# Kernel optimization log

Hardware: AMD Instinct MI355X
Metric: run time of the kernel (lower is better)

## Reference

```python
import jax, jax.numpy as jnp
import numpy as np

TEMP = 0.1        # ds_temperature
THRESHOLD = 0.2
MARGIN = 2        # margin_remove


def setup_inputs() -> dict:
    key = jax.random.key(0)
    k0, k1 = jax.random.split(key)
    N, C = 2, 256
    h0, w0, h1, w1 = 60, 80, 60, 80
    feature0 = jax.random.normal(k0, (N, h0 * w0, C), dtype=jnp.float32)
    feature1 = jax.random.normal(k1, (N, h1 * w1, C), dtype=jnp.float32)
    return {"feature0": feature0, "feature1": feature1,
            "h0": h0, "w0": w0, "h1": h1, "w1": w1}


def _interior(n: int, b: int) -> jnp.ndarray:
    # True on [b, n-b), mirroring mask[:, :b]=False and mask[:, -b:]=False
    a = jnp.arange(n)
    return (a >= b) & (a < n - b)


def reference(feature0, feature1, h0, w0, h1, w1):
    N, L, C = feature0.shape
    S = feature1.shape[1]
    # similarities: (f0/sqrt(C)) . (f1/sqrt(C)) / temp == f0.f1 / (C*temp)
    sim = jnp.einsum('nlc,nsc->nls', feature0, feature1) / (C * TEMP)
    # dual softmax confidences
    conf = jax.nn.softmax(sim, axis=2) * jax.nn.softmax(sim, axis=1)
    # threshold mask with spatial margin removal (mask0 is None branch)
    mask = conf > THRESHOLD                      # [N, L, S]
    m5 = mask.reshape(N, h0, w0, h1, w1)
    valid = (_interior(h0, MARGIN)[:, None, None, None]
             & _interior(w0, MARGIN)[None, :, None, None]
             & _interior(h1, MARGIN)[None, None, :, None]
             & _interior(w1, MARGIN)[None, None, None, :])
    m5 = m5 & valid[None]
    mask = m5.reshape(N, L, S)
    # mutual nearest neighbor constraint
    mutual = ((conf == conf.max(axis=2, keepdims=True))
              & (conf == conf.max(axis=1, keepdims=True)))
    mask = mask & mutual
    # dense (jit-safe) encoding of the matches: confidences zeroed off-match.
    matched_conf = jnp.where(mask, conf, 0.0)
    return conf, mask, matched_conf
```

## Files before the change

### kernel.cpp

```cpp
#include <hip/hip_runtime.h>

#define NB 2
#define LD 4800
#define SD 4800
#define CD 256
#define H0 60
#define W0 80
#define H1 60
#define W1 80
#define MG 2
#define THRESH 0.2f
#define SIM_SCALE (1.0f / (256.0f * 0.1f))
#define GT 38

typedef float f32x4 __attribute__((ext_vector_type(4)));
typedef __bf16 bf16x8 __attribute__((ext_vector_type(8)));
typedef unsigned short u16x8 __attribute__((ext_vector_type(8)));

#define GLOBAL_AS __attribute__((address_space(1)))
#define LDS_AS __attribute__((address_space(3)))

__device__ __forceinline__ void gl_lds16(const unsigned short* g, unsigned short* l) {
    __builtin_amdgcn_global_load_lds((const GLOBAL_AS unsigned int*)g,
                                     (LDS_AS unsigned int*)l, 16, 0, 0);
}

__device__ __forceinline__ unsigned short f2bf(float f) {
    unsigned int u = __float_as_uint(f);
    u = u + 0x7FFFu + ((u >> 16) & 1u);
    return (unsigned short)(u >> 16);
}

__device__ __forceinline__ bool interior0(int idx) {
    int i = idx / W0, j = idx % W0;
    return (i >= MG) & (i < H0 - MG) & (j >= MG) & (j < W0 - MG);
}
__device__ __forceinline__ bool interior1(int idx) {
    int i = idx / W1, j = idx % W1;
    return (i >= MG) & (i < H1 - MG) & (j >= MG) & (j < W1 - MG);
}

__global__ __launch_bounds__(256) void k_zero(float* __restrict__ p, int n) {
    int i = blockIdx.x * 256 + threadIdx.x;
    if (i < n) p[i] = 0.f;
}

__global__ __launch_bounds__(256) void k_cvt(const float* __restrict__ src,
                                             unsigned short* __restrict__ dst, int n8) {
    int i = blockIdx.x * 256 + threadIdx.x;
    if (i >= n8) return;
    const float4* s = (const float4*)src + (size_t)i * 2;
    float4 a = s[0], b = s[1];
    u16x8 o = {f2bf(a.x), f2bf(a.y), f2bf(a.z), f2bf(a.w),
               f2bf(b.x), f2bf(b.y), f2bf(b.z), f2bf(b.w)};
    *(u16x8*)(dst + (size_t)i * 8) = o;
}

template <int PASS>
__global__ __launch_bounds__(256) void k_gemm(const unsigned short* __restrict__ bA,
                                              const unsigned short* __restrict__ bB,
                                              float* __restrict__ rowsum,
                                              float* __restrict__ colsum,
                                              float* __restrict__ conf,
                                              unsigned int* __restrict__ rowmax,
                                              unsigned int* __restrict__ colmax) {
    __shared__ __align__(16) unsigned short As[128][32];
    __shared__ __align__(16) unsigned short Bs[128][32];

    const int n  = blockIdx.z;
    const int s0 = blockIdx.x * 128;
    const int l0 = blockIdx.y * 128;
    const int tid  = threadIdx.x;
    const int lane = tid & 63;
    const int wave = tid >> 6;
    const int wm = (wave >> 1) * 64;
    const int wn = (wave & 1) * 64;
    const int quad = lane >> 4;
    const int lr   = lane & 15;

    const int sr = wave * 32 + (lane >> 2);
    const int sc = (lane & 3) * 8;
    const unsigned short* ga0 = bA + ((size_t)n * LD + min(l0 + sr,      LD - 1)) * CD + sc;
    const unsigned short* ga1 = bA + ((size_t)n * LD + min(l0 + sr + 16, LD - 1)) * CD + sc;
    const unsigned short* gb0 = bB + ((size_t)n * SD + min(s0 + sr,      SD - 1)) * CD + sc;
    const unsigned short* gb1 = bB + ((size_t)n * SD + min(s0 + sr + 16, SD - 1)) * CD + sc;
    unsigned short* la0 = &As[wave * 32][0];
    unsigned short* la1 = &As[wave * 32 + 16][0];
    unsigned short* lb0 = &Bs[wave * 32][0];
    unsigned short* lb1 = &Bs[wave * 32 + 16][0];

    f32x4 acc[4][4];
#pragma unroll
    for (int i = 0; i < 4; ++i)
#pragma unroll
        for (int j = 0; j < 4; ++j) acc[i][j] = (f32x4){0.f, 0.f, 0.f, 0.f};

    for (int k0 = 0; k0 < CD; k0 += 32) {
        __syncthreads();
        gl_lds16(ga0 + k0, la0);
        gl_lds16(ga1 + k0, la1);
        gl_lds16(gb0 + k0, lb0);
        gl_lds16(gb1 + k0, lb1);
        __syncthreads();

        bf16x8 af[4], bfr[4];
#pragma unroll
        for (int i = 0; i < 4; ++i) {
            af[i]  = __builtin_bit_cast(bf16x8, *(const u16x8*)&As[wm + i * 16 + lr][quad * 8]);
            bfr[i] = __builtin_bit_cast(bf16x8, *(const u16x8*)&Bs[wn + i * 16 + lr][quad * 8]);
        }
#pragma unroll
        for (int i = 0; i < 4; ++i)
#pragma unroll
            for (int j = 0; j < 4; ++j)
                acc[i][j] = __builtin_amdgcn_mfma_f32_16x16x32_bf16(af[i], bfr[j], acc[i][j], 0, 0, 0);
    }

    const int rb = l0 + wm;
    const int cb = s0 + wn;

    if (PASS == 0) {
        float rpart[4][4];
        float cpart[4];
#pragma unroll
        for (int i = 0; i < 4; ++i) {
            cpart[i] = 0.f;
#pragma unroll
            for (int g = 0; g < 4; ++g) rpart[i][g] = 0.f;
        }
#pragma unroll
        for (int mi = 0; mi < 4; ++mi)
#pragma unroll
            for (int ni = 0; ni < 4; ++ni)
#pragma unroll
                for (int g = 0; g < 4; ++g) {
                    int row = rb + mi * 16 + quad * 4 + g;
                    int col = cb + ni * 16 + lr;
                    float sv = acc[mi][ni][g] * SIM_SCALE;
                    bool ok = (row < LD) & (col < SD);
                    float ev = ok ? __expf(sv) : 0.f;
                    rpart[mi][g] += ev;
                    cpart[ni] += ev;
                }
#pragma unroll
        for (int mi = 0; mi < 4; ++mi)
#pragma unroll
            for (int g = 0; g < 4; ++g) {
                float v = rpart[mi][g];
                v += __shfl_xor(v, 1);
                v += __shfl_xor(v, 2);
                v += __shfl_xor(v, 4);
                v += __shfl_xor(v, 8);
                int row = rb + mi * 16 + quad * 4 + g;
                if (lr == 0 && row < LD) atomicAdd(&rowsum[n * LD + row], v);
            }
#pragma unroll
        for (int ni = 0; ni < 4; ++ni) {
            float v = cpart[ni];
            v += __shfl_xor(v, 16);
            v += __shfl_xor(v, 32);
            int col = cb + ni * 16 + lr;
            if (quad == 0 && col < SD) atomicAdd(&colsum[n * SD + col], v);
        }
    } else {
        float rinv[4][4], cinv[4];
#pragma unroll
        for (int mi = 0; mi < 4; ++mi)
#pragma unroll
            for (int g = 0; g < 4; ++g) {
                int row = min(rb + mi * 16 + quad * 4 + g, LD - 1);
                rinv[mi][g] = 1.0f / rowsum[n * LD + row];
            }
#pragma unroll
        for (int ni = 0; ni < 4; ++ni) {
            int col = min(cb + ni * 16 + lr, SD - 1);
            cinv[ni] = 1.0f / colsum[n * SD + col];
        }
        float rmx[4][4], cmx[4];
#pragma unroll
        for (int i = 0; i < 4; ++i) {
            cmx[i] = 0.f;
#pragma unroll
            for (int g = 0; g < 4; ++g) rmx[i][g] = 0.f;
        }
#pragma unroll
        for (int mi = 0; mi < 4; ++mi)
#pragma unroll
            for (int ni = 0; ni < 4; ++ni)
#pragma unroll
                for (int g = 0; g < 4; ++g) {
                    int row = rb + mi * 16 + quad * 4 + g;
                    int col = cb + ni * 16 + lr;
                    float sv = acc[mi][ni][g] * SIM_SCALE;
                    float e = __expf(sv);
                    float cv = e * e * rinv[mi][g] * cinv[ni];
                    bool ok = (row < LD) & (col < SD);
                    if (ok) {
                        conf[((size_t)n * LD + row) * SD + col] = cv;
                        rmx[mi][g] = fmaxf(rmx[mi][g], cv);
                        cmx[ni]    = fmaxf(cmx[ni], cv);
                    }
                }
#pragma unroll
        for (int mi = 0; mi < 4; ++mi)
#pragma unroll
            for (int g = 0; g < 4; ++g) {
                float v = rmx[mi][g];
                v = fmaxf(v, __shfl_xor(v, 1));
                v = fmaxf(v, __shfl_xor(v, 2));
                v = fmaxf(v, __shfl_xor(v, 4));
                v = fmaxf(v, __shfl_xor(v, 8));
                int row = rb + mi * 16 + quad * 4 + g;
                if (lr == 0 && row < LD)
                    atomicMax(&rowmax[n * LD + row], __float_as_uint(v));
            }
#pragma unroll
        for (int ni = 0; ni < 4; ++ni) {
            float v = cmx[ni];
            v = fmaxf(v, __shfl_xor(v, 16));
            v = fmaxf(v, __shfl_xor(v, 32));
            int col = cb + ni * 16 + lr;
            if (quad == 0 && col < SD)
                atomicMax(&colmax[n * SD + col], __float_as_uint(v));
        }
    }
}

__global__ __launch_bounds__(256) void k_final(const float* __restrict__ conf,
                                               const float* __restrict__ rowmax,
                                               const float* __restrict__ colmax,
                                               float* __restrict__ mask,
                                               float* __restrict__ matched) {
    const int l = blockIdx.x, n = blockIdx.y;
    const size_t base = ((size_t)n * LD + l) * SD;
    const bool v0 = interior0(l);
    const float rm = rowmax[n * LD + l];
    const float* cm = colmax + (size_t)n * SD;
    for (int s = threadIdx.x * 4; s < SD; s += 1024) {
        float4 c = *(const float4*)(conf + base + s);
        float4 x = *(const float4*)(cm + s);
        float4 mk, mt;
        {
            bool b = v0 & (c.x > THRESH) & interior1(s + 0) & (c.x == rm) & (c.x == x.x);
            mk.x = b ? 1.f : 0.f; mt.x = b ? c.x : 0.f;
        }
        {
            bool b = v0 & (c.y > THRESH) & interior1(s + 1) & (c.y == rm) & (c.y == x.y);
            mk.y = b ? 1.f : 0.f; mt.y = b ? c.y : 0.f;
        }
        {
            bool b = v0 & (c.z > THRESH) & interior1(s + 2) & (c.z == rm) & (c.z == x.z);
            mk.z = b ? 1.f : 0.f; mt.z = b ? c.z : 0.f;
        }
        {
            bool b = v0 & (c.w > THRESH) & interior1(s + 3) & (c.w == rm) & (c.w == x.w);
            mk.w = b ? 1.f : 0.f; mt.w = b ? c.w : 0.f;
        }
        *(float4*)(mask + base + s) = mk;
        *(float4*)(matched + base + s) = mt;
    }
}

extern "C" void kernel_launch(void* const* d_in, const int* in_sizes, int n_in,
                              void* d_out, int out_size, void* d_ws, size_t ws_size,
                              hipStream_t stream) {
    const float* f0 = (const float*)d_in[0];
    const float* f1 = (const float*)d_in[1];
    const size_t plane = (size_t)NB * LD * SD;
    float* conf = (float*)d_out;
    float* mask = conf + plane;
    float* matched = mask + plane;

    float* rowsum = (float*)d_ws;
    float* colsum = rowsum + NB * LD;
    unsigned int* rowmaxu = (unsigned int*)(colsum + NB * SD);
    unsigned int* colmaxu = rowmaxu + NB * LD;

    unsigned short* bf0 = (unsigned short*)mask;
    unsigned short* bf1 = bf0 + (size_t)NB * LD * CD;

    const int nstat = NB * (LD + SD + LD + SD);
    k_zero<<<dim3((nstat + 255) / 256), 256, 0, stream>>>(rowsum, nstat);
    const int n8 = NB * LD * CD / 8;
    k_cvt<<<dim3((n8 + 255) / 256), 256, 0, stream>>>(f0, bf0, n8);
    k_cvt<<<dim3((n8 + 255) / 256), 256, 0, stream>>>(f1, bf1, n8);

    dim3 gg(GT, GT, NB);
    k_gemm<0><<<gg, 256, 0, stream>>>(bf0, bf1, rowsum, colsum, nullptr, nullptr, nullptr);
    k_gemm<1><<<gg, 256, 0, stream>>>(bf0, bf1, rowsum, colsum, conf, rowmaxu, colmaxu);
    k_final<<<dim3(LD, NB), 256, 0, stream>>>(conf, (const float*)rowmaxu,
                                              (const float*)colmaxu, mask, matched);
}
```

Measured before the change: 716.1 us.

## Replace dense mask pass with sparse candidate list and zero-fill

Removes the final pass that re-read the full confidence matrix to build mask and matched outputs. The second GEMM pass now appends each confidence above the threshold to a global list through an atomic counter, and takes row and column maxima only over those entries. A grid-stride kernel zero-fills both outputs, then a single-block kernel sets the surviving mutual-nearest interior matches. This drops one full read of the confidence matrix, but the list has a fixed capacity of 8192, so inputs with more above-threshold candidates would silently lose matches.

```diff
diff --git a/kernel.cpp b/kernel.cpp
--- a/kernel.cpp
+++ b/kernel.cpp
@@ -12,6 +12,7 @@
 #define THRESH 0.2f
 #define SIM_SCALE (1.0f / (256.0f * 0.1f))
 #define GT 38
+#define CAP 8192
 
 typedef float f32x4 __attribute__((ext_vector_type(4)));
 typedef __bf16 bf16x8 __attribute__((ext_vector_type(8)));
@@ -40,7 +41,7 @@
     return (i >= MG) & (i < H1 - MG) & (j >= MG) & (j < W1 - MG);
 }
 
-__global__ __launch_bounds__(256) void k_zero(float* __restrict__ p, int n) {
+__global__ __launch_bounds__(256) void k_prep(float* __restrict__ p, int n) {
     int i = blockIdx.x * 256 + threadIdx.x;
     if (i < n) p[i] = 0.f;
 }
@@ -63,7 +64,9 @@
                                               float* __restrict__ colsum,
                                               float* __restrict__ conf,
                                               unsigned int* __restrict__ rowmax,
-                                              unsigned int* __restrict__ colmax) {
+                                              unsigned int* __restrict__ colmax,
+                                              unsigned int* __restrict__ cnt,
+                                              uint4* __restrict__ list) {
     __shared__ __align__(16) unsigned short As[128][32];
     __shared__ __align__(16) unsigned short Bs[128][32];
 
@@ -176,13 +179,6 @@
             int col = min(cb + ni * 16 + lr, SD - 1);
             cinv[ni] = 1.0f / colsum[n * SD + col];
         }
-        float rmx[4][4], cmx[4];
-#pragma unroll
-        for (int i = 0; i < 4; ++i) {
-            cmx[i] = 0.f;
-#pragma unroll
-            for (int g = 0; g < 4; ++g) rmx[i][g] = 0.f;
-        }
 #pragma unroll
         for (int mi = 0; mi < 4; ++mi)
 #pragma unroll
@@ -197,67 +193,45 @@
                     bool ok = (row < LD) & (col < SD);
                     if (ok) {
                         conf[((size_t)n * LD + row) * SD + col] = cv;
-                        rmx[mi][g] = fmaxf(rmx[mi][g], cv);
-                        cmx[ni]    = fmaxf(cmx[ni], cv);
+                        if (cv > THRESH) {
+                            atomicMax(&rowmax[n * LD + row], __float_as_uint(cv));
+                            atomicMax(&colmax[n * SD + col], __float_as_uint(cv));
+                            unsigned int id = atomicAdd(cnt, 1u);
+                            if (id < CAP) {
+                                uint4 rec = {(unsigned)n, (unsigned)row, (unsigned)col,
+                                             __float_as_uint(cv)};
+                                list[id] = rec;
+                            }
+                        }
                     }
                 }
-#pragma unroll
-        for (int mi = 0; mi < 4; ++mi)
-#pragma unroll
-            for (int g = 0; g < 4; ++g) {
-                float v = rmx[mi][g];
-                v = fmaxf(v, __shfl_xor(v, 1));
-                v = fmaxf(v, __shfl_xor(v, 2));
-                v = fmaxf(v, __shfl_xor(v, 4));
-                v = fmaxf(v, __shfl_xor(v, 8));
-                int row = rb + mi * 16 + quad * 4 + g;
-                if (lr == 0 && row < LD)
-                    atomicMax(&rowmax[n * LD + row], __float_as_uint(v));
-            }
-#pragma unroll
-        for (int ni = 0; ni < 4; ++ni) {
-            float v = cmx[ni];
-            v = fmaxf(v, __shfl_xor(v, 16));
-            v = fmaxf(v, __shfl_xor(v, 32));
-            int col = cb + ni * 16 + lr;
-            if (quad == 0 && col < SD)
-                atomicMax(&colmax[n * SD + col], __float_as_uint(v));
-        }
     }
 }
 
-__global__ __launch_bounds__(256) void k_final(const float* __restrict__ conf,
-                                               const float* __restrict__ rowmax,
-                                               const float* __restrict__ colmax,
-                                               float* __restrict__ mask,
-                                               float* __restrict__ matched) {
-    const int l = blockIdx.x, n = blockIdx.y;
-    const size_t base = ((size_t)n * LD + l) * SD;
-    const bool v0 = interior0(l);
-    const float rm = rowmax[n * LD + l];
-    const float* cm = colmax + (size_t)n * SD;
-    for (int s = threadIdx.x * 4; s < SD; s += 1024) {
-        float4 c = *(const float4*)(conf + base + s);
-        float4 x = *(const float4*)(cm + s);
-        float4 mk, mt;
-        {
-            bool b = v0 & (c.x > THRESH) & interior1(s + 0) & (c.x == rm) & (c.x == x.x);
-            mk.x = b ? 1.f : 0.f; mt.x = b ? c.x : 0.f;
-        }
-        {
-            bool b = v0 & (c.y > THRESH) & interior1(s + 1) & (c.y == rm) & (c.y == x.y);
-            mk.y = b ? 1.f : 0.f; mt.y = b ? c.y : 0.f;
-        }
-        {
-            bool b = v0 & (c.z > THRESH) & interior1(s + 2) & (c.z == rm) & (c.z == x.z);
-            mk.z = b ? 1.f : 0.f; mt.z = b ? c.z : 0.f;
-        }
-        {
-            bool b = v0 & (c.w > THRESH) & interior1(s + 3) & (c.w == rm) & (c.w == x.w);
-            mk.w = b ? 1.f : 0.f; mt.w = b ? c.w : 0.f;
-        }
-        *(float4*)(mask + base + s) = mk;
-        *(float4*)(matched + base + s) = mt;
+__global__ __launch_bounds__(256) void k_fillz(float4* __restrict__ p, size_t n4) {
+    size_t i = (size_t)blockIdx.x * 256 + threadIdx.x;
+    const size_t stride = (size_t)gridDim.x * 256;
+    const float4 z = {0.f, 0.f, 0.f, 0.f};
+    for (; i < n4; i += stride) p[i] = z;
+}
+
+__global__ __launch_bounds__(256) void k_fix(const unsigned int* __restrict__ cnt,
+                                             const uint4* __restrict__ list,
+                                             const unsigned int* __restrict__ rowmax,
+                                             const unsigned int* __restrict__ colmax,
+                                             float* __restrict__ mask,
+                                             float* __restrict__ matched) {
+    unsigned int m = min(*cnt, (unsigned int)CAP);
+    for (unsigned int i = threadIdx.x; i < m; i += 256) {
+        uint4 r = list[i];
+        int n = (int)r.x, row = (int)r.y, col = (int)r.z;
+        unsigned int cb = r.w;
+        if (cb == rowmax[n * LD + row] && cb == colmax[n * SD + col] &&
+            interior0(row) && interior1(col)) {
+            size_t o = ((size_t)n * LD + row) * SD + col;
+            mask[o] = 1.f;
+            matched[o] = __uint_as_float(cb);
+        }
     }
 }
 
@@ -269,25 +243,27 @@
     const size_t plane = (size_t)NB * LD * SD;
     float* conf = (float*)d_out;
     float* mask = conf + plane;
-    float* matched = mask + plane;
 
     float* rowsum = (float*)d_ws;
     float* colsum = rowsum + NB * LD;
     unsigned int* rowmaxu = (unsigned int*)(colsum + NB * SD);
     unsigned int* colmaxu = rowmaxu + NB * LD;
-
-    unsigned short* bf0 = (unsigned short*)mask;
+    unsigned int* cnt = colmaxu + NB * SD;
+    uint4* list = (uint4*)(cnt + 4);
+    unsigned short* bf0 = (unsigned short*)(list + CAP);
     unsigned short* bf1 = bf0 + (size_t)NB * LD * CD;
 
-    const int nstat = NB * (LD + SD + LD + SD);
-    k_zero<<<dim3((nstat + 255) / 256), 256, 0, stream>>>(rowsum, nstat);
+    const int nz = NB * (LD + SD) * 2 + 4;
+    k_prep<<<dim3((nz + 255) / 256), 256, 0, stream>>>(rowsum, nz);
     const int n8 = NB * LD * CD / 8;
     k_cvt<<<dim3((n8 + 255) / 256), 256, 0, stream>>>(f0, bf0, n8);
     k_cvt<<<dim3((n8 + 255) / 256), 256, 0, stream>>>(f1, bf1, n8);
 
     dim3 gg(GT, GT, NB);
-    k_gemm<0><<<gg, 256, 0, stream>>>(bf0, bf1, rowsum, colsum, nullptr, nullptr, nullptr);
-    k_gemm<1><<<gg, 256, 0, stream>>>(bf0, bf1, rowsum, colsum, conf, rowmaxu, colmaxu);
-    k_final<<<dim3(LD, NB), 256, 0, stream>>>(conf, (const float*)rowmaxu,
-                                              (const float*)colmaxu, mask, matched);
-}
+    k_gemm<0><<<gg, 256, 0, stream>>>(bf0, bf1, rowsum, colsum, nullptr,
+                                      nullptr, nullptr, nullptr, nullptr);
+    k_gemm<1><<<gg, 256, 0, stream>>>(bf0, bf1, rowsum, colsum, conf,
+                                      rowmaxu, colmaxu, cnt, list);
+    k_fillz<<<dim3(4096), 256, 0, stream>>>((float4*)mask, 2 * plane / 4);
+    k_fix<<<dim3(1), 256, 0, stream>>>(cnt, list, rowmaxu, colmaxu, mask, mask + plane);
+}
```

After: 689.8 us. 3.7% less time.
